# Optimization experiments

Measured on AMD Instinct MI355X. Metric: run time of the kernel, lower is better.

The kernel has to match this reference:

```python
import jax, jax.numpy as jnp
import numpy as np

B, N, E = 2, 2048, 1024
H, D = 16, 64  # context_dim = H*D = 1024


def setup_inputs() -> dict:
    key = jax.random.key(0)
    ks = jax.random.split(key, 6)
    s = 0.02
    return {
        "input_emb": jax.random.normal(ks[0], (B, N, E), dtype=jnp.float32),
        "Wq": jax.random.normal(ks[1], (E, H * D), dtype=jnp.float32) * s,
        "Wk": jax.random.normal(ks[2], (E, D), dtype=jnp.float32) * s,
        "Wv": jax.random.normal(ks[3], (E, D), dtype=jnp.float32) * s,
        "Wo": jax.random.normal(ks[4], (H * D, H * D), dtype=jnp.float32) * s,
        "bo": jax.random.normal(ks[5], (H * D,), dtype=jnp.float32) * s,
    }


def reference(input_emb, Wq, Wk, Wv, Wo, bo):
    b, n, _ = input_emb.shape
    Q = (input_emb @ Wq).reshape(b, n, H, D)          # (B,N,H,D)
    K = input_emb @ Wk                                 # (B,N,D) shared across heads (MQA)
    V = input_emb @ Wv                                 # (B,N,D)
    # scores: (B,H,N,N); mask is applied before scaling in the torch code,
    # but -inf/scale == -inf so mask-then-scale == scale-then-mask.
    scores = jnp.einsum("bnhd,bmd->bhnm", Q, K) / jnp.sqrt(jnp.float32(D))
    causal = jnp.tril(jnp.ones((n, n), dtype=bool))    # True = keep
    scores = jnp.where(causal[None, None], scores, -jnp.inf)
    weights = jax.nn.softmax(scores, axis=-1)          # dropout rate 0.0 -> identity
    Z = jnp.einsum("bhnm,bmd->bnhd", weights, V).reshape(b, n, H * D)
    return Z @ Wo + bo
```

## Files before the change

kernel.cpp:

```cpp
#include <hip/hip_runtime.h>
#include <hip/hip_bf16.h>


#define NQ 2048
#define BATCH 2
#define HEADS 16
#define HD 64
#define EMB 1024
#define NKV 1152

typedef short s16x8 __attribute__((ext_vector_type(8)));
typedef float f32x4 __attribute__((ext_vector_type(4)));
typedef unsigned short ushort_t;

__device__ __forceinline__ ushort_t f2bf(float f) {
    unsigned u = __builtin_bit_cast(unsigned, f);
    u += 0x7fff + ((u >> 16) & 1);
    return (ushort_t)(u >> 16);
}

__device__ __forceinline__ void store_out(float* p, float v) { *p = v; }
__device__ __forceinline__ void store_out(ushort_t* p, float v) { *p = f2bf(v); }

#define GL16(g, l)                                                                  \
    __builtin_amdgcn_global_load_lds(                                               \
        (const __attribute__((address_space(1))) unsigned int*)(g),                 \
        (__attribute__((address_space(3))) unsigned int*)(l), 16, 0, 0)

__global__ __launch_bounds__(256) void prep(const float* __restrict__ x,
                                            const float* __restrict__ Wq,
                                            const float* __restrict__ Wk,
                                            const float* __restrict__ Wv,
                                            const float* __restrict__ Wo,
                                            ushort_t* __restrict__ xb,
                                            ushort_t* __restrict__ Wqkv_t,
                                            ushort_t* __restrict__ Wo_t) {
    const int bid = blockIdx.x, t = threadIdx.x;
    if (bid < 4096) {
        const int i = bid * 1024 + t * 4;
        const float4 v = *(const float4*)&x[i];
        ushort_t o[4] = {f2bf(v.x), f2bf(v.y), f2bf(v.z), f2bf(v.w)};
        *(uint2*)&xb[i] = *(uint2*)o;
        return;
    }
    int tb = bid - 4096;
    const float* src; ushort_t* dst; int N, n0, k0;
    if (tb < 1024)      { src = Wq; N = 1024; dst = Wqkv_t;
                          n0 = (tb & 31) * 32; k0 = (tb >> 5) * 32; }
    else if (tb < 1088) { tb -= 1024; src = Wk; N = 64; dst = Wqkv_t + (size_t)1024 * EMB;
                          n0 = (tb & 1) * 32; k0 = (tb >> 1) * 32; }
    else if (tb < 1152) { tb -= 1088; src = Wv; N = 64; dst = Wqkv_t + (size_t)1088 * EMB;
                          n0 = (tb & 1) * 32; k0 = (tb >> 1) * 32; }
    else                { tb -= 1152; src = Wo; N = 1024; dst = Wo_t;
                          n0 = (tb & 31) * 32; k0 = (tb >> 5) * 32; }
    __shared__ float tile[32][33];
    const int tx = t & 31, ty = t >> 5;
#pragma unroll
    for (int i = 0; i < 32; i += 8)
        tile[ty + i][tx] = src[(size_t)(k0 + ty + i) * N + n0 + tx];
    __syncthreads();
#pragma unroll
    for (int i = 0; i < 32; i += 8)
        dst[(size_t)(n0 + ty + i) * EMB + k0 + tx] = f2bf(tile[tx][ty + i]);
}

template<bool HAS_BIAS, bool WRITE_VT, typename OutT>
__global__ __launch_bounds__(256) void gemm_bf16(const ushort_t* __restrict__ A,
                                                 const ushort_t* __restrict__ Bt,
                                                 const float* __restrict__ bias,
                                                 OutT* __restrict__ C,
                                                 ushort_t* __restrict__ Vt,
                                                 int M, int N, int K) {
    __shared__ __align__(16) ushort_t Al[64 * 32];
    __shared__ __align__(16) ushort_t Bl[128 * 32];
    const int t = threadIdx.x;
    const int w = t >> 6, lane = t & 63, quad = lane >> 4, ln = lane & 15;
    const int row0 = blockIdx.y * 64, col0 = blockIdx.x * 128;

    const int rA = t >> 2;
    const int lcA = (t & 3) ^ ((rA >> 1) & 3);
    const int rB1 = 64 + rA;
    const ushort_t* ga  = A  + (size_t)(row0 + rA) * K + lcA * 8;
    const ushort_t* gb0 = Bt + (size_t)(col0 + rA) * K + lcA * 8;
    const ushort_t* gb1 = Bt + (size_t)(col0 + rB1) * K + lcA * 8;
    ushort_t* lA  = Al + w * 512;
    ushort_t* lB0 = Bl + w * 512;
    ushort_t* lB1 = Bl + 2048 + w * 512;

    f32x4 acc[4][2] = {};
    const int sw = (ln >> 1) & 3;
    for (int k0 = 0; k0 < K; k0 += 32) {
        GL16(ga, lA); GL16(gb0, lB0); GL16(gb1, lB1);
        ga += 32; gb0 += 32; gb1 += 32;
        __syncthreads();

        s16x8 af[4], bf[2];
#pragma unroll
        for (int mt = 0; mt < 4; ++mt)
            af[mt] = *(const s16x8*)&Al[(mt * 16 + ln) * 32 + ((quad ^ sw) * 8)];
#pragma unroll
        for (int nt = 0; nt < 2; ++nt)
            bf[nt] = *(const s16x8*)&Bl[(w * 32 + nt * 16 + ln) * 32 + ((quad ^ sw) * 8)];
#pragma unroll
        for (int mt = 0; mt < 4; ++mt)
#pragma unroll
            for (int nt = 0; nt < 2; ++nt)
                acc[mt][nt] = __builtin_amdgcn_mfma_f32_16x16x32_bf16(
                    af[mt], bf[nt], acc[mt][nt], 0, 0, 0);
        __syncthreads();
    }

#pragma unroll
    for (int nt = 0; nt < 2; ++nt) {
        const int col = col0 + w * 32 + nt * 16 + ln;
        const float bv = HAS_BIAS ? bias[col] : 0.f;
#pragma unroll
        for (int mt = 0; mt < 4; ++mt) {
#pragma unroll
            for (int r = 0; r < 4; ++r) {
                const int row = row0 + mt * 16 + quad * 4 + r;
                store_out(&C[(size_t)row * N + col], acc[mt][nt][r] + bv);
            }
            if (WRITE_VT && col >= 1088) {
                const int d = col - 1088;
                const int n = row0 + mt * 16 + quad * 4;
                const int bb = n >> 11, nn = n & 2047;
                ushort_t tmp[4] = {f2bf(acc[mt][nt][0]), f2bf(acc[mt][nt][1]),
                                   f2bf(acc[mt][nt][2]), f2bf(acc[mt][nt][3])};
                *(uint2*)&Vt[((size_t)bb * 64 + d) * NQ + nn] = *(uint2*)tmp;
            }
        }
    }
}

__device__ __forceinline__ void stage_tile(ushort_t* lds, const ushort_t* g,
                                           size_t rstride, int w, int lane) {
#pragma unroll
    for (int it = 0; it < 2; ++it) {
        const int u = (w * 2 + it) * 64 + lane;
        const int row = u >> 3, pc = u & 7;
        const int lc = pc ^ (row & 7);
        GL16(g + (size_t)row * rstride + lc * 8, lds + (size_t)(w * 2 + it) * 512);
    }
}

__device__ __forceinline__ s16x8 frag(const ushort_t* lds, int row, int lc) {
    const int phys = lc ^ (row & 7);
    return *(const s16x8*)&lds[row * 64 + phys * 8];
}

__global__ __launch_bounds__(256, 4) void attn_mfma(const ushort_t* __restrict__ QKV,
                                                    const ushort_t* __restrict__ Vt,
                                                    ushort_t* __restrict__ Z) {
    const int bid = blockIdx.x;
    const int b = (bid >> 4) & 1, h = bid & 15;
    const int i = bid >> 5, k = i >> 3, j = i & 7;
    const int qt = (k == 0) ? 2 * j : (k == 1) ? 31 - 2 * j
                 : (k == 2) ? 2 * j + 1 : 30 - 2 * j;
    const int t = threadIdx.x;
    const int w = t >> 6, lane = t & 63, quad = lane >> 4, ln = lane & 15;

    __shared__ __align__(16) ushort_t QPs[64 * 64];
    __shared__ __align__(16) ushort_t Kl[2][64 * 64];
    __shared__ __align__(16) ushort_t Vl[2][64 * 64];

    const ushort_t* Kg = QKV + (size_t)b * NQ * NKV + 1024;
    const ushort_t* Vg = Vt + (size_t)b * 64 * NQ;

    stage_tile(QPs, QKV + (size_t)(b * NQ + qt * 64) * NKV + h * HD, NKV, w, lane);
    stage_tile(Kl[0], Kg, NKV, w, lane);
    stage_tile(Vl[0], Vg, NQ, w, lane);
    __syncthreads();

    const s16x8 aQ0 = frag(QPs, w * 16 + ln, quad);
    const s16x8 aQ1 = frag(QPs, w * 16 + ln, 4 + quad);

    f32x4 o[4];
#pragma unroll
    for (int ii = 0; ii < 4; ++ii) o[ii] = f32x4{0.f, 0.f, 0.f, 0.f};
    float mrow[4], lrow[4];
#pragma unroll
    for (int r = 0; r < 4; ++r) { mrow[r] = -1e30f; lrow[r] = 0.f; }

#pragma unroll 1
    for (int jt = 0; jt <= qt; ++jt) {
        const int cur = jt & 1;
        if (jt < qt) {
            stage_tile(Kl[cur ^ 1], Kg + (size_t)(jt + 1) * 64 * NKV, NKV, w, lane);
            stage_tile(Vl[cur ^ 1], Vg + (jt + 1) * 64, NQ, w, lane);
        }
        const ushort_t* Kc = Kl[cur];
        const ushort_t* Vc = Vl[cur];

        f32x4 s[4];
#pragma unroll
        for (int nt = 0; nt < 4; ++nt) {
            f32x4 acc = f32x4{0.f, 0.f, 0.f, 0.f};
            const s16x8 b0 = frag(Kc, nt * 16 + ln, quad);
            const s16x8 b1 = frag(Kc, nt * 16 + ln, 4 + quad);
            acc = __builtin_amdgcn_mfma_f32_16x16x32_bf16(aQ0, b0, acc, 0, 0, 0);
            acc = __builtin_amdgcn_mfma_f32_16x16x32_bf16(aQ1, b1, acc, 0, 0, 0);
            s[nt] = acc;
        }

        const bool diag = (jt == qt);
        float rmax[4];
#pragma unroll
        for (int r = 0; r < 4; ++r) rmax[r] = -1e30f;
#pragma unroll
        for (int nt = 0; nt < 4; ++nt)
#pragma unroll
            for (int r = 0; r < 4; ++r) {
                float v = s[nt][r] * 0.125f;
                if (diag && (nt * 16 + ln) > (w * 16 + quad * 4 + r)) v = -1e30f;
                s[nt][r] = v;
                rmax[r] = fmaxf(rmax[r], v);
            }
#pragma unroll
        for (int r = 0; r < 4; ++r) {
            rmax[r] = fmaxf(rmax[r], __shfl_xor(rmax[r], 1));
            rmax[r] = fmaxf(rmax[r], __shfl_xor(rmax[r], 2));
            rmax[r] = fmaxf(rmax[r], __shfl_xor(rmax[r], 4));
            rmax[r] = fmaxf(rmax[r], __shfl_xor(rmax[r], 8));
        }
        float alpha[4], rsum[4];
#pragma unroll
        for (int r = 0; r < 4; ++r) {
            const float mnew = fmaxf(mrow[r], rmax[r]);
            alpha[r] = __expf(mrow[r] - mnew);
            mrow[r] = mnew;
            rsum[r] = 0.f;
        }
#pragma unroll
        for (int nt = 0; nt < 4; ++nt)
#pragma unroll
            for (int r = 0; r < 4; ++r) {
                const float pv = __expf(s[nt][r] - mrow[r]);
                s[nt][r] = pv;
                rsum[r] += pv;
            }
#pragma unroll
        for (int r = 0; r < 4; ++r) {
            rsum[r] += __shfl_xor(rsum[r], 1);
            rsum[r] += __shfl_xor(rsum[r], 2);
            rsum[r] += __shfl_xor(rsum[r], 4);
            rsum[r] += __shfl_xor(rsum[r], 8);
            lrow[r] = lrow[r] * alpha[r] + rsum[r];
        }
#pragma unroll
        for (int ntd = 0; ntd < 4; ++ntd)
#pragma unroll
            for (int r = 0; r < 4; ++r) o[ntd][r] *= alpha[r];

#pragma unroll
        for (int nt = 0; nt < 4; ++nt)
#pragma unroll
            for (int r = 0; r < 4; ++r) {
                const int prow = quad * 4 + r;
                const int pc = (nt * 2 + (ln >> 3)) ^ (prow & 7);
                QPs[(w * 16 + prow) * 64 + pc * 8 + (ln & 7)] = f2bf(s[nt][r]);
            }
        asm volatile("s_waitcnt lgkmcnt(0)" ::: "memory");

        const s16x8 aP0 = frag(QPs, w * 16 + ln, quad);
        const s16x8 aP1 = frag(QPs, w * 16 + ln, 4 + quad);
#pragma unroll
        for (int ntd = 0; ntd < 4; ++ntd) {
            const s16x8 b0 = frag(Vc, ntd * 16 + ln, quad);
            const s16x8 b1 = frag(Vc, ntd * 16 + ln, 4 + quad);
            o[ntd] = __builtin_amdgcn_mfma_f32_16x16x32_bf16(aP0, b0, o[ntd], 0, 0, 0);
            o[ntd] = __builtin_amdgcn_mfma_f32_16x16x32_bf16(aP1, b1, o[ntd], 0, 0, 0);
        }
        __syncthreads();
    }

    float invl[4];
#pragma unroll
    for (int r = 0; r < 4; ++r) invl[r] = 1.f / lrow[r];
#pragma unroll
    for (int ntd = 0; ntd < 4; ++ntd)
#pragma unroll
        for (int r = 0; r < 4; ++r) {
            const size_t row = (size_t)(b * NQ + qt * 64 + w * 16 + quad * 4 + r);
            Z[row * EMB + h * HD + ntd * 16 + ln] = f2bf(o[ntd][r] * invl[r]);
        }
}

extern "C" void kernel_launch(void* const* d_in, const int* in_sizes, int n_in,
                              void* d_out, int out_size, void* d_ws, size_t ws_size,
                              hipStream_t stream) {
    const float* x  = (const float*)d_in[0];
    const float* Wq = (const float*)d_in[1];
    const float* Wk = (const float*)d_in[2];
    const float* Wv = (const float*)d_in[3];
    const float* Wo = (const float*)d_in[4];
    const float* bo = (const float*)d_in[5];
    float* out = (float*)d_out;

    const int M = BATCH * NQ;
    char* ws = (char*)d_ws;
    ushort_t* xb     = (ushort_t*)ws;
    ushort_t* Wqkv_t = (ushort_t*)(ws + (size_t)8  * 1024 * 1024);
    ushort_t* Wo_t   = (ushort_t*)(ws + (size_t)11 * 1024 * 1024);
    ushort_t* QKV    = (ushort_t*)(ws + (size_t)13 * 1024 * 1024);
    ushort_t* Vt     = (ushort_t*)(ws + (size_t)23 * 1024 * 1024);
    ushort_t* Zb     = (ushort_t*)(ws + (size_t)24 * 1024 * 1024);

    dim3 blk(256);
    prep<<<dim3(6272), blk, 0, stream>>>(x, Wq, Wk, Wv, Wo, xb, Wqkv_t, Wo_t);
    gemm_bf16<false, true, ushort_t><<<dim3(NKV / 128, M / 64), blk, 0, stream>>>(
        xb, Wqkv_t, nullptr, QKV, Vt, M, NKV, EMB);
    attn_mfma<<<dim3(1024), blk, 0, stream>>>(QKV, Vt, Zb);
    gemm_bf16<true, false, float><<<dim3(EMB / 128, M / 64), blk, 0, stream>>>(
        Zb, Wo_t, bo, out, nullptr, M, EMB, EMB);
}
```

Measured before the change: 188.6 us.

## Load K/V fragments directly from global into registers, drop LDS staging

The attention kernel stops staging Q, K and V tiles through double-buffered shared memory. Each wave now loads its MFMA operand fragments straight from global memory (relying on L2/cache reuse across the four waves) and keeps only a per-wave P scratch buffer in LDS. Because P is per-wave, the block-wide __syncthreads per key tile is removed. The trade is less LDS and no block barriers against four-times-redundant global/L2 traffic for K and V and no prefetch overlap.

```diff
diff --git a/kernel.cpp b/kernel.cpp
--- a/kernel.cpp
+++ b/kernel.cpp
@@ -133,17 +133,6 @@
     }
 }
 
-__device__ __forceinline__ void stage_tile(ushort_t* lds, const ushort_t* g,
-                                           size_t rstride, int w, int lane) {
-#pragma unroll
-    for (int it = 0; it < 2; ++it) {
-        const int u = (w * 2 + it) * 64 + lane;
-        const int row = u >> 3, pc = u & 7;
-        const int lc = pc ^ (row & 7);
-        GL16(g + (size_t)row * rstride + lc * 8, lds + (size_t)(w * 2 + it) * 512);
-    }
-}
-
 __device__ __forceinline__ s16x8 frag(const ushort_t* lds, int row, int lc) {
     const int phys = lc ^ (row & 7);
     return *(const s16x8*)&lds[row * 64 + phys * 8];
@@ -160,20 +149,16 @@
     const int t = threadIdx.x;
     const int w = t >> 6, lane = t & 63, quad = lane >> 4, ln = lane & 15;
 
-    __shared__ __align__(16) ushort_t QPs[64 * 64];
-    __shared__ __align__(16) ushort_t Kl[2][64 * 64];
-    __shared__ __align__(16) ushort_t Vl[2][64 * 64];
+    __shared__ __align__(16) ushort_t Ps[4 * 16 * 64];
 
     const ushort_t* Kg = QKV + (size_t)b * NQ * NKV + 1024;
     const ushort_t* Vg = Vt + (size_t)b * 64 * NQ;
-
-    stage_tile(QPs, QKV + (size_t)(b * NQ + qt * 64) * NKV + h * HD, NKV, w, lane);
-    stage_tile(Kl[0], Kg, NKV, w, lane);
-    stage_tile(Vl[0], Vg, NQ, w, lane);
-    __syncthreads();
-
-    const s16x8 aQ0 = frag(QPs, w * 16 + ln, quad);
-    const s16x8 aQ1 = frag(QPs, w * 16 + ln, 4 + quad);
+    ushort_t* Pw = Ps + w * 1024;
+
+    const ushort_t* qrow =
+        QKV + (size_t)(b * NQ + qt * 64 + w * 16 + ln) * NKV + h * HD;
+    const s16x8 aQ0 = *(const s16x8*)(qrow + quad * 8);
+    const s16x8 aQ1 = *(const s16x8*)(qrow + 32 + quad * 8);
 
     f32x4 o[4];
 #pragma unroll
@@ -184,23 +169,29 @@
 
 #pragma unroll 1
     for (int jt = 0; jt <= qt; ++jt) {
-        const int cur = jt & 1;
-        if (jt < qt) {
-            stage_tile(Kl[cur ^ 1], Kg + (size_t)(jt + 1) * 64 * NKV, NKV, w, lane);
-            stage_tile(Vl[cur ^ 1], Vg + (jt + 1) * 64, NQ, w, lane);
-        }
-        const ushort_t* Kc = Kl[cur];
-        const ushort_t* Vc = Vl[cur];
+        const ushort_t* kb = Kg + (size_t)(jt * 64 + ln) * NKV + quad * 8;
+        s16x8 kf0[4], kf1[4];
+#pragma unroll
+        for (int nt = 0; nt < 4; ++nt) {
+            kf0[nt] = *(const s16x8*)(kb + (size_t)(nt * 16) * NKV);
+            kf1[nt] = *(const s16x8*)(kb + (size_t)(nt * 16) * NKV + 32);
+        }
 
         f32x4 s[4];
 #pragma unroll
         for (int nt = 0; nt < 4; ++nt) {
             f32x4 acc = f32x4{0.f, 0.f, 0.f, 0.f};
-            const s16x8 b0 = frag(Kc, nt * 16 + ln, quad);
-            const s16x8 b1 = frag(Kc, nt * 16 + ln, 4 + quad);
-            acc = __builtin_amdgcn_mfma_f32_16x16x32_bf16(aQ0, b0, acc, 0, 0, 0);
-            acc = __builtin_amdgcn_mfma_f32_16x16x32_bf16(aQ1, b1, acc, 0, 0, 0);
+            acc = __builtin_amdgcn_mfma_f32_16x16x32_bf16(aQ0, kf0[nt], acc, 0, 0, 0);
+            acc = __builtin_amdgcn_mfma_f32_16x16x32_bf16(aQ1, kf1[nt], acc, 0, 0, 0);
             s[nt] = acc;
+        }
+
+        const ushort_t* vb = Vg + (size_t)ln * NQ + jt * 64 + quad * 8;
+        s16x8 vf0[4], vf1[4];
+#pragma unroll
+        for (int ntd = 0; ntd < 4; ++ntd) {
+            vf0[ntd] = *(const s16x8*)(vb + (size_t)(ntd * 16) * NQ);
+            vf1[ntd] = *(const s16x8*)(vb + (size_t)(ntd * 16) * NQ + 32);
         }
 
         const bool diag = (jt == qt);
@@ -258,20 +249,17 @@
             for (int r = 0; r < 4; ++r) {
                 const int prow = quad * 4 + r;
                 const int pc = (nt * 2 + (ln >> 3)) ^ (prow & 7);
-                QPs[(w * 16 + prow) * 64 + pc * 8 + (ln & 7)] = f2bf(s[nt][r]);
+                Pw[prow * 64 + pc * 8 + (ln & 7)] = f2bf(s[nt][r]);
             }
         asm volatile("s_waitcnt lgkmcnt(0)" ::: "memory");
 
-        const s16x8 aP0 = frag(QPs, w * 16 + ln, quad);
-        const s16x8 aP1 = frag(QPs, w * 16 + ln, 4 + quad);
+        const s16x8 aP0 = frag(Pw, ln, quad);
+        const s16x8 aP1 = frag(Pw, ln, 4 + quad);
 #pragma unroll
         for (int ntd = 0; ntd < 4; ++ntd) {
-            const s16x8 b0 = frag(Vc, ntd * 16 + ln, quad);
-            const s16x8 b1 = frag(Vc, ntd * 16 + ln, 4 + quad);
-            o[ntd] = __builtin_amdgcn_mfma_f32_16x16x32_bf16(aP0, b0, o[ntd], 0, 0, 0);
-            o[ntd] = __builtin_amdgcn_mfma_f32_16x16x32_bf16(aP1, b1, o[ntd], 0, 0, 0);
-        }
-        __syncthreads();
+            o[ntd] = __builtin_amdgcn_mfma_f32_16x16x32_bf16(aP0, vf0[ntd], o[ntd], 0, 0, 0);
+            o[ntd] = __builtin_amdgcn_mfma_f32_16x16x32_bf16(aP1, vf1[ntd], o[ntd], 0, 0, 0);
+        }
     }
 
     float invl[4];
```

Result: slower. 247.1 us (+31.0%).

## Enlarge GEMM tiles to 128x128 and attention query tiles to 128 rows

Applied to the files above, without the earlier changes.

The GEMM now computes a 128x128 output tile per block, with a 2x2 wave grid each holding a 64x64 sub-tile, so each loaded A and B fragment feeds more MFMAs. Attention blocks now use 512 threads covering 128 query rows, so each staged K/V tile is shared by twice as many queries. The old interleaved query-tile ordering is replaced by a descending qt order. This halves the grid sizes and raises register pressure and per-block LDS, which can reduce occupancy and worsen load balance on the causal triangle.

```diff
diff --git a/kernel.cpp b/kernel.cpp
--- a/kernel.cpp
+++ b/kernel.cpp
@@ -71,59 +71,67 @@
                                                  OutT* __restrict__ C,
                                                  ushort_t* __restrict__ Vt,
                                                  int M, int N, int K) {
-    __shared__ __align__(16) ushort_t Al[64 * 32];
+    __shared__ __align__(16) ushort_t Al[128 * 32];
     __shared__ __align__(16) ushort_t Bl[128 * 32];
     const int t = threadIdx.x;
     const int w = t >> 6, lane = t & 63, quad = lane >> 4, ln = lane & 15;
-    const int row0 = blockIdx.y * 64, col0 = blockIdx.x * 128;
-
-    const int rA = t >> 2;
-    const int lcA = (t & 3) ^ ((rA >> 1) & 3);
-    const int rB1 = 64 + rA;
-    const ushort_t* ga  = A  + (size_t)(row0 + rA) * K + lcA * 8;
-    const ushort_t* gb0 = Bt + (size_t)(col0 + rA) * K + lcA * 8;
-    const ushort_t* gb1 = Bt + (size_t)(col0 + rB1) * K + lcA * 8;
-    ushort_t* lA  = Al + w * 512;
+    const int wm = w >> 1, wn = w & 1;
+    const int row0 = blockIdx.y * 128, col0 = blockIdx.x * 128;
+
+    const int r0 = t >> 2, r1 = (t + 256) >> 2;
+    const int lc0 = (t & 3) ^ ((r0 >> 1) & 3);
+    const int lc1 = (t & 3) ^ ((r1 >> 1) & 3);
+    const ushort_t* ga0 = A + (size_t)(row0 + r0) * K + lc0 * 8;
+    const ushort_t* ga1 = A + (size_t)(row0 + r1) * K + lc1 * 8;
+    const ushort_t* gb0 = Bt + (size_t)(col0 + r0) * K + lc0 * 8;
+    const ushort_t* gb1 = Bt + (size_t)(col0 + r1) * K + lc1 * 8;
+    ushort_t* lA0 = Al + w * 512;
+    ushort_t* lA1 = Al + 2048 + w * 512;
     ushort_t* lB0 = Bl + w * 512;
     ushort_t* lB1 = Bl + 2048 + w * 512;
 
-    f32x4 acc[4][2] = {};
+    f32x4 acc[4][4] = {};
     const int sw = (ln >> 1) & 3;
     for (int k0 = 0; k0 < K; k0 += 32) {
-        GL16(ga, lA); GL16(gb0, lB0); GL16(gb1, lB1);
-        ga += 32; gb0 += 32; gb1 += 32;
+        GL16(ga0, lA0); GL16(ga1, lA1);
+        GL16(gb0, lB0); GL16(gb1, lB1);
+        ga0 += 32; ga1 += 32; gb0 += 32; gb1 += 32;
         __syncthreads();
 
-        s16x8 af[4], bf[2];
+        s16x8 af[4], bf[4];
+#pragma unroll
+        for (int mt = 0; mt < 4; ++mt) {
+            const int r = wm * 64 + mt * 16 + ln;
+            af[mt] = *(const s16x8*)&Al[r * 32 + ((quad ^ sw) * 8)];
+        }
+#pragma unroll
+        for (int nt = 0; nt < 4; ++nt) {
+            const int r = wn * 64 + nt * 16 + ln;
+            bf[nt] = *(const s16x8*)&Bl[r * 32 + ((quad ^ sw) * 8)];
+        }
 #pragma unroll
         for (int mt = 0; mt < 4; ++mt)
-            af[mt] = *(const s16x8*)&Al[(mt * 16 + ln) * 32 + ((quad ^ sw) * 8)];
-#pragma unroll
-        for (int nt = 0; nt < 2; ++nt)
-            bf[nt] = *(const s16x8*)&Bl[(w * 32 + nt * 16 + ln) * 32 + ((quad ^ sw) * 8)];
-#pragma unroll
-        for (int mt = 0; mt < 4; ++mt)
-#pragma unroll
-            for (int nt = 0; nt < 2; ++nt)
+#pragma unroll
+            for (int nt = 0; nt < 4; ++nt)
                 acc[mt][nt] = __builtin_amdgcn_mfma_f32_16x16x32_bf16(
                     af[mt], bf[nt], acc[mt][nt], 0, 0, 0);
         __syncthreads();
     }
 
 #pragma unroll
-    for (int nt = 0; nt < 2; ++nt) {
-        const int col = col0 + w * 32 + nt * 16 + ln;
+    for (int nt = 0; nt < 4; ++nt) {
+        const int col = col0 + wn * 64 + nt * 16 + ln;
         const float bv = HAS_BIAS ? bias[col] : 0.f;
 #pragma unroll
         for (int mt = 0; mt < 4; ++mt) {
 #pragma unroll
             for (int r = 0; r < 4; ++r) {
-                const int row = row0 + mt * 16 + quad * 4 + r;
+                const int row = row0 + wm * 64 + mt * 16 + quad * 4 + r;
                 store_out(&C[(size_t)row * N + col], acc[mt][nt][r] + bv);
             }
             if (WRITE_VT && col >= 1088) {
                 const int d = col - 1088;
-                const int n = row0 + mt * 16 + quad * 4;
+                const int n = row0 + wm * 64 + mt * 16 + quad * 4;
                 const int bb = n >> 11, nn = n & 2047;
                 ushort_t tmp[4] = {f2bf(acc[mt][nt][0]), f2bf(acc[mt][nt][1]),
                                    f2bf(acc[mt][nt][2]), f2bf(acc[mt][nt][3])};
@@ -133,14 +141,23 @@
     }
 }
 
-__device__ __forceinline__ void stage_tile(ushort_t* lds, const ushort_t* g,
-                                           size_t rstride, int w, int lane) {
+__device__ __forceinline__ void stage64(ushort_t* lds, const ushort_t* g,
+                                        size_t rstride, int t) {
+    const int row = t >> 3, pc = t & 7;
+    const int lc = pc ^ (row & 7);
+    GL16(g + (size_t)row * rstride + lc * 8, lds + (size_t)(t >> 3 << 3) * 8
+                                                + 0 * 0 + (size_t)0 + ((size_t)(t & ~63)) * 8);
+}
+
+
+__device__ __forceinline__ void stage128(ushort_t* lds, const ushort_t* g,
+                                         size_t rstride, int t) {
 #pragma unroll
     for (int it = 0; it < 2; ++it) {
-        const int u = (w * 2 + it) * 64 + lane;
+        const int u = it * 512 + t;
         const int row = u >> 3, pc = u & 7;
         const int lc = pc ^ (row & 7);
-        GL16(g + (size_t)row * rstride + lc * 8, lds + (size_t)(w * 2 + it) * 512);
+        GL16(g + (size_t)row * rstride + lc * 8, lds + (size_t)(u & ~63) * 8);
     }
 }
 
@@ -149,31 +166,34 @@
     return *(const s16x8*)&lds[row * 64 + phys * 8];
 }
 
-__global__ __launch_bounds__(256, 4) void attn_mfma(const ushort_t* __restrict__ QKV,
+__global__ __launch_bounds__(512, 6) void attn_mfma(const ushort_t* __restrict__ QKV,
                                                     const ushort_t* __restrict__ Vt,
                                                     ushort_t* __restrict__ Z) {
     const int bid = blockIdx.x;
-    const int b = (bid >> 4) & 1, h = bid & 15;
-    const int i = bid >> 5, k = i >> 3, j = i & 7;
-    const int qt = (k == 0) ? 2 * j : (k == 1) ? 31 - 2 * j
-                 : (k == 2) ? 2 * j + 1 : 30 - 2 * j;
+    const int qt = 15 - (bid >> 5);
+    const int rem = bid & 31, b = rem >> 4, h = rem & 15;
     const int t = threadIdx.x;
     const int w = t >> 6, lane = t & 63, quad = lane >> 4, ln = lane & 15;
 
-    __shared__ __align__(16) ushort_t QPs[64 * 64];
+    __shared__ __align__(16) ushort_t QPs[128 * 64];
     __shared__ __align__(16) ushort_t Kl[2][64 * 64];
     __shared__ __align__(16) ushort_t Vl[2][64 * 64];
 
     const ushort_t* Kg = QKV + (size_t)b * NQ * NKV + 1024;
     const ushort_t* Vg = Vt + (size_t)b * 64 * NQ;
 
-    stage_tile(QPs, QKV + (size_t)(b * NQ + qt * 64) * NKV + h * HD, NKV, w, lane);
-    stage_tile(Kl[0], Kg, NKV, w, lane);
-    stage_tile(Vl[0], Vg, NQ, w, lane);
+    stage128(QPs, QKV + (size_t)(b * NQ + qt * 128) * NKV + h * HD, NKV, t);
+    {
+        const int row = t >> 3, pc = t & 7;
+        const int lc = pc ^ (row & 7);
+        GL16(Kg + (size_t)row * NKV + lc * 8, Kl[0] + (size_t)(t & ~63) * 8);
+        GL16(Vg + (size_t)row * NQ + lc * 8, Vl[0] + (size_t)(t & ~63) * 8);
+    }
     __syncthreads();
 
     const s16x8 aQ0 = frag(QPs, w * 16 + ln, quad);
     const s16x8 aQ1 = frag(QPs, w * 16 + ln, 4 + quad);
+    ushort_t* Pw = QPs;
 
     f32x4 o[4];
 #pragma unroll
@@ -182,12 +202,17 @@
 #pragma unroll
     for (int r = 0; r < 4; ++r) { mrow[r] = -1e30f; lrow[r] = 0.f; }
 
+    const int niter = 2 * qt + 2;
 #pragma unroll 1
-    for (int jt = 0; jt <= qt; ++jt) {
+    for (int jt = 0; jt < niter; ++jt) {
         const int cur = jt & 1;
-        if (jt < qt) {
-            stage_tile(Kl[cur ^ 1], Kg + (size_t)(jt + 1) * 64 * NKV, NKV, w, lane);
-            stage_tile(Vl[cur ^ 1], Vg + (jt + 1) * 64, NQ, w, lane);
+        if (jt + 1 < niter) {
+            const int row = t >> 3, pc = t & 7;
+            const int lc = pc ^ (row & 7);
+            GL16(Kg + (size_t)((jt + 1) * 64 + row) * NKV + lc * 8,
+                 Kl[cur ^ 1] + (size_t)(t & ~63) * 8);
+            GL16(Vg + (size_t)row * NQ + (jt + 1) * 64 + lc * 8,
+                 Vl[cur ^ 1] + (size_t)(t & ~63) * 8);
         }
         const ushort_t* Kc = Kl[cur];
         const ushort_t* Vc = Vl[cur];
@@ -203,7 +228,7 @@
             s[nt] = acc;
         }
 
-        const bool diag = (jt == qt);
+        const bool diag = (jt >= 2 * qt);
         float rmax[4];
 #pragma unroll
         for (int r = 0; r < 4; ++r) rmax[r] = -1e30f;
@@ -212,7 +237,8 @@
 #pragma unroll
             for (int r = 0; r < 4; ++r) {
                 float v = s[nt][r] * 0.125f;
-                if (diag && (nt * 16 + ln) > (w * 16 + quad * 4 + r)) v = -1e30f;
+                if (diag && (jt * 64 + nt * 16 + ln) >
+                            (qt * 128 + w * 16 + quad * 4 + r)) v = -1e30f;
                 s[nt][r] = v;
                 rmax[r] = fmaxf(rmax[r], v);
             }
@@ -258,12 +284,12 @@
             for (int r = 0; r < 4; ++r) {
                 const int prow = quad * 4 + r;
                 const int pc = (nt * 2 + (ln >> 3)) ^ (prow & 7);
-                QPs[(w * 16 + prow) * 64 + pc * 8 + (ln & 7)] = f2bf(s[nt][r]);
+                Pw[(w * 16 + prow) * 64 + pc * 8 + (ln & 7)] = f2bf(s[nt][r]);
             }
         asm volatile("s_waitcnt lgkmcnt(0)" ::: "memory");
 
-        const s16x8 aP0 = frag(QPs, w * 16 + ln, quad);
-        const s16x8 aP1 = frag(QPs, w * 16 + ln, 4 + quad);
+        const s16x8 aP0 = frag(Pw, w * 16 + ln, quad);
+        const s16x8 aP1 = frag(Pw, w * 16 + ln, 4 + quad);
 #pragma unroll
         for (int ntd = 0; ntd < 4; ++ntd) {
             const s16x8 b0 = frag(Vc, ntd * 16 + ln, quad);
@@ -281,7 +307,7 @@
     for (int ntd = 0; ntd < 4; ++ntd)
 #pragma unroll
         for (int r = 0; r < 4; ++r) {
-            const size_t row = (size_t)(b * NQ + qt * 64 + w * 16 + quad * 4 + r);
+            const size_t row = (size_t)(b * NQ + qt * 128 + w * 16 + quad * 4 + r);
             Z[row * EMB + h * HD + ntd * 16 + ln] = f2bf(o[ntd][r] * invl[r]);
         }
 }
@@ -306,11 +332,10 @@
     ushort_t* Vt     = (ushort_t*)(ws + (size_t)23 * 1024 * 1024);
     ushort_t* Zb     = (ushort_t*)(ws + (size_t)24 * 1024 * 1024);
 
-    dim3 blk(256);
-    prep<<<dim3(6272), blk, 0, stream>>>(x, Wq, Wk, Wv, Wo, xb, Wqkv_t, Wo_t);
-    gemm_bf16<false, true, ushort_t><<<dim3(NKV / 128, M / 64), blk, 0, stream>>>(
+    prep<<<dim3(6272), dim3(256), 0, stream>>>(x, Wq, Wk, Wv, Wo, xb, Wqkv_t, Wo_t);
+    gemm_bf16<false, true, ushort_t><<<dim3(NKV / 128, M / 128), dim3(256), 0, stream>>>(
         xb, Wqkv_t, nullptr, QKV, Vt, M, NKV, EMB);
-    attn_mfma<<<dim3(1024), blk, 0, stream>>>(QKV, Vt, Zb);
-    gemm_bf16<true, false, float><<<dim3(EMB / 128, M / 64), blk, 0, stream>>>(
+    attn_mfma<<<dim3(512), dim3(512), 0, stream>>>(QKV, Vt, Zb);
+    gemm_bf16<true, false, float><<<dim3(EMB / 128, M / 128), dim3(256), 0, stream>>>(
         Zb, Wo_t, bo, out, nullptr, M, EMB, EMB);
 }
```

New measurement: 253.4 us. 34.3% more time.

## Use 128-row query tiles with 8 waves per attention block

Applied to the files above, without the earlier changes.

The attention kernel now gives each block 128 query rows instead of 64, using 512 threads (8 waves). Each staged K/V tile is therefore shared by twice as many query rows, which halves K/V global traffic and LDS staging per query. The grid becomes 512 blocks with a simpler two-group tile ordering to balance the causal workload. Fewer, larger blocks may reduce occupancy and load-balance granularity, and the diagonal masking now covers two KV tiles per block.

```diff
diff --git a/kernel.cpp b/kernel.cpp
--- a/kernel.cpp
+++ b/kernel.cpp
@@ -133,47 +133,47 @@
     }
 }
 
-__device__ __forceinline__ void stage_tile(ushort_t* lds, const ushort_t* g,
-                                           size_t rstride, int w, int lane) {
-#pragma unroll
-    for (int it = 0; it < 2; ++it) {
-        const int u = (w * 2 + it) * 64 + lane;
-        const int row = u >> 3, pc = u & 7;
-        const int lc = pc ^ (row & 7);
-        GL16(g + (size_t)row * rstride + lc * 8, lds + (size_t)(w * 2 + it) * 512);
-    }
-}
-
 __device__ __forceinline__ s16x8 frag(const ushort_t* lds, int row, int lc) {
     const int phys = lc ^ (row & 7);
     return *(const s16x8*)&lds[row * 64 + phys * 8];
 }
 
-__global__ __launch_bounds__(256, 4) void attn_mfma(const ushort_t* __restrict__ QKV,
+__global__ __launch_bounds__(512, 4) void attn_mfma(const ushort_t* __restrict__ QKV,
                                                     const ushort_t* __restrict__ Vt,
                                                     ushort_t* __restrict__ Z) {
     const int bid = blockIdx.x;
-    const int b = (bid >> 4) & 1, h = bid & 15;
-    const int i = bid >> 5, k = i >> 3, j = i & 7;
-    const int qt = (k == 0) ? 2 * j : (k == 1) ? 31 - 2 * j
-                 : (k == 2) ? 2 * j + 1 : 30 - 2 * j;
+    const int grp = bid >> 8, c = bid & 255;
+    const int qt = grp ? (c >> 5) : 15 - (c >> 5);
+    const int b = (c >> 4) & 1, h = c & 15;
     const int t = threadIdx.x;
     const int w = t >> 6, lane = t & 63, quad = lane >> 4, ln = lane & 15;
 
-    __shared__ __align__(16) ushort_t QPs[64 * 64];
+    __shared__ __align__(16) ushort_t QPs[128 * 64];
     __shared__ __align__(16) ushort_t Kl[2][64 * 64];
     __shared__ __align__(16) ushort_t Vl[2][64 * 64];
 
     const ushort_t* Kg = QKV + (size_t)b * NQ * NKV + 1024;
     const ushort_t* Vg = Vt + (size_t)b * 64 * NQ;
 
-    stage_tile(QPs, QKV + (size_t)(b * NQ + qt * 64) * NKV + h * HD, NKV, w, lane);
-    stage_tile(Kl[0], Kg, NKV, w, lane);
-    stage_tile(Vl[0], Vg, NQ, w, lane);
+    {
+#pragma unroll
+        for (int it = 0; it < 2; ++it) {
+            const int u = it * 512 + t;
+            const int row = u >> 3, pc = u & 7;
+            const int lc = pc ^ (row & 7);
+            GL16(QKV + (size_t)(b * NQ + qt * 128 + row) * NKV + h * HD + lc * 8,
+                 QPs + (size_t)(u & ~63) * 8);
+        }
+        const int row = t >> 3, pc = t & 7;
+        const int lc = pc ^ (row & 7);
+        GL16(Kg + (size_t)row * NKV + lc * 8, Kl[0] + (size_t)(t & ~63) * 8);
+        GL16(Vg + (size_t)row * NQ + lc * 8, Vl[0] + (size_t)(t & ~63) * 8);
+    }
     __syncthreads();
 
     const s16x8 aQ0 = frag(QPs, w * 16 + ln, quad);
     const s16x8 aQ1 = frag(QPs, w * 16 + ln, 4 + quad);
+    ushort_t* Pw = QPs;
 
     f32x4 o[4];
 #pragma unroll
@@ -182,12 +182,17 @@
 #pragma unroll
     for (int r = 0; r < 4; ++r) { mrow[r] = -1e30f; lrow[r] = 0.f; }
 
+    const int niter = 2 * qt + 2;
 #pragma unroll 1
-    for (int jt = 0; jt <= qt; ++jt) {
+    for (int jt = 0; jt < niter; ++jt) {
         const int cur = jt & 1;
-        if (jt < qt) {
-            stage_tile(Kl[cur ^ 1], Kg + (size_t)(jt + 1) * 64 * NKV, NKV, w, lane);
-            stage_tile(Vl[cur ^ 1], Vg + (jt + 1) * 64, NQ, w, lane);
+        if (jt + 1 < niter) {
+            const int row = t >> 3, pc = t & 7;
+            const int lc = pc ^ (row & 7);
+            GL16(Kg + (size_t)((jt + 1) * 64 + row) * NKV + lc * 8,
+                 Kl[cur ^ 1] + (size_t)(t & ~63) * 8);
+            GL16(Vg + (size_t)row * NQ + (jt + 1) * 64 + lc * 8,
+                 Vl[cur ^ 1] + (size_t)(t & ~63) * 8);
         }
         const ushort_t* Kc = Kl[cur];
         const ushort_t* Vc = Vl[cur];
@@ -203,7 +208,7 @@
             s[nt] = acc;
         }
 
-        const bool diag = (jt == qt);
+        const bool diag = (jt >= 2 * qt);
         float rmax[4];
 #pragma unroll
         for (int r = 0; r < 4; ++r) rmax[r] = -1e30f;
@@ -212,7 +217,8 @@
 #pragma unroll
             for (int r = 0; r < 4; ++r) {
                 float v = s[nt][r] * 0.125f;
-                if (diag && (nt * 16 + ln) > (w * 16 + quad * 4 + r)) v = -1e30f;
+                if (diag && (jt * 64 + nt * 16 + ln) >
+                            (qt * 128 + w * 16 + quad * 4 + r)) v = -1e30f;
                 s[nt][r] = v;
                 rmax[r] = fmaxf(rmax[r], v);
             }
@@ -258,12 +264,12 @@
             for (int r = 0; r < 4; ++r) {
                 const int prow = quad * 4 + r;
                 const int pc = (nt * 2 + (ln >> 3)) ^ (prow & 7);
-                QPs[(w * 16 + prow) * 64 + pc * 8 + (ln & 7)] = f2bf(s[nt][r]);
+                Pw[(w * 16 + prow) * 64 + pc * 8 + (ln & 7)] = f2bf(s[nt][r]);
             }
         asm volatile("s_waitcnt lgkmcnt(0)" ::: "memory");
 
-        const s16x8 aP0 = frag(QPs, w * 16 + ln, quad);
-        const s16x8 aP1 = frag(QPs, w * 16 + ln, 4 + quad);
+        const s16x8 aP0 = frag(Pw, w * 16 + ln, quad);
+        const s16x8 aP1 = frag(Pw, w * 16 + ln, 4 + quad);
 #pragma unroll
         for (int ntd = 0; ntd < 4; ++ntd) {
             const s16x8 b0 = frag(Vc, ntd * 16 + ln, quad);
@@ -281,7 +287,7 @@
     for (int ntd = 0; ntd < 4; ++ntd)
 #pragma unroll
         for (int r = 0; r < 4; ++r) {
-            const size_t row = (size_t)(b * NQ + qt * 64 + w * 16 + quad * 4 + r);
+            const size_t row = (size_t)(b * NQ + qt * 128 + w * 16 + quad * 4 + r);
             Z[row * EMB + h * HD + ntd * 16 + ln] = f2bf(o[ntd][r] * invl[r]);
         }
 }
@@ -306,11 +312,10 @@
     ushort_t* Vt     = (ushort_t*)(ws + (size_t)23 * 1024 * 1024);
     ushort_t* Zb     = (ushort_t*)(ws + (size_t)24 * 1024 * 1024);
 
-    dim3 blk(256);
-    prep<<<dim3(6272), blk, 0, stream>>>(x, Wq, Wk, Wv, Wo, xb, Wqkv_t, Wo_t);
-    gemm_bf16<false, true, ushort_t><<<dim3(NKV / 128, M / 64), blk, 0, stream>>>(
+    prep<<<dim3(6272), dim3(256), 0, stream>>>(x, Wq, Wk, Wv, Wo, xb, Wqkv_t, Wo_t);
+    gemm_bf16<false, true, ushort_t><<<dim3(NKV / 128, M / 64), dim3(256), 0, stream>>>(
         xb, Wqkv_t, nullptr, QKV, Vt, M, NKV, EMB);
-    attn_mfma<<<dim3(1024), blk, 0, stream>>>(QKV, Vt, Zb);
-    gemm_bf16<true, false, float><<<dim3(EMB / 128, M / 64), blk, 0, stream>>>(
+    attn_mfma<<<dim3(512), dim3(512), 0, stream>>>(QKV, Vt, Zb);
+    gemm_bf16<true, false, float><<<dim3(EMB / 128, M / 64), dim3(256), 0, stream>>>(
         Zb, Wo_t, bo, out, nullptr, M, EMB, EMB);
 }
```

After: 194.6 us. 3.2% more time.
